# Kernel optimization log

Hardware: AMD Instinct MI355X
Metric: run time of the kernel (lower is better)

## Reference

```python
import jax, jax.numpy as jnp
import numpy as np

B, S, D, H = 2, 2048, 1024, 16
DK = D // H  # 64
THETA = 10000.0
SCALE = 1.0 / np.sqrt(DK)


def _rope(t, pos):
    """Apply rotary embedding. t: [b,h,s,dk], pos: [b,s] int."""
    inv_freq = THETA ** (-jnp.arange(0, DK, 2, dtype=jnp.float32) / DK)  # [dk/2]
    ang = pos[:, None, :, None].astype(jnp.float32) * inv_freq  # [b,1,s,dk/2]
    cos, sin = jnp.cos(ang), jnp.sin(ang)
    t1, t2 = t[..., 0::2], t[..., 1::2]  # interleaved pairs
    rot = jnp.stack([t1 * cos - t2 * sin, t1 * sin + t2 * cos], axis=-1)
    return rot.reshape(t.shape)


def setup_inputs() -> dict:
    key = jax.random.key(0)
    ks = jax.random.split(key, 9)
    sc = 0.02
    x = jax.random.normal(ks[0], (B, S, D), jnp.float32)
    token_position = jnp.tile(jnp.arange(S, dtype=jnp.int32)[None, :], (B, 1))
    Wq = jax.random.normal(ks[1], (D, D), jnp.float32) * sc
    Wk = jax.random.normal(ks[2], (D, D), jnp.float32) * sc
    Wv = jax.random.normal(ks[3], (D, D), jnp.float32) * sc
    Wo = jax.random.normal(ks[4], (D, D), jnp.float32) * sc
    bq = jnp.zeros((D,), jnp.float32)
    bk = jnp.zeros((D,), jnp.float32)
    bv = jnp.zeros((D,), jnp.float32)
    bo = jnp.zeros((D,), jnp.float32)
    return {"x": x, "token_position": token_position,
            "Wq": Wq, "bq": bq, "Wk": Wk, "bk": bk,
            "Wv": Wv, "bv": bv, "Wo": Wo, "bo": bo}


def reference(x, token_position, Wq, bq, Wk, bk, Wv, bv, Wo, bo):
    b, s, d = x.shape
    # projections, split heads: [b,s,d] -> [b,h,s,dk]
    def heads(t):
        return t.reshape(b, s, H, DK).transpose(0, 2, 1, 3)
    q = heads(x @ Wq + bq)
    k = heads(x @ Wk + bk)
    v = heads(x @ Wv + bv)
    q = _rope(q, token_position)
    k = _rope(k, token_position)
    scores = jnp.einsum('bhnk,bhmk->bhnm', q, k) * SCALE  # [b,h,s,s]
    causal = jnp.tril(jnp.ones((s, s), dtype=bool))
    scores = jnp.where(causal, scores, -jnp.inf)
    probs = jax.nn.softmax(scores, axis=-1)
    o = jnp.einsum('bhnm,bhmk->bhnk', probs, v)  # [b,h,s,dk]
    o = o.transpose(0, 2, 1, 3).reshape(b, s, d)
    return o @ Wo + bo
```

## Files before the change

kernel.cpp:

```cpp
#include <hip/hip_runtime.h>
#include <math.h>

#define BB  2
#define SS  2048
#define DD  1024
#define HH  16
#define DKK 64

constexpr float kScale = 0.125f;
constexpr float kC1 = 0.18033688011112042f;
constexpr float kC2 = 23.0831206542234144f;

typedef __bf16 bf16x8 __attribute__((ext_vector_type(8)));
typedef float f32x4 __attribute__((ext_vector_type(4)));

__device__ __forceinline__ void async_copy16(const void* g, void* l) {
  __builtin_amdgcn_global_load_lds(
      (const __attribute__((address_space(1))) void*)g,
      (__attribute__((address_space(3))) void*)l, 16, 0, 0);
}

__global__ __launch_bounds__(256) void prep_kernel(
    const float* __restrict__ x, const int* __restrict__ pos,
    const float* __restrict__ W0, const float* __restrict__ W1,
    const float* __restrict__ W2, const float* __restrict__ W3,
    __bf16* __restrict__ xb, float2* __restrict__ rtab,
    __bf16* __restrict__ T0, __bf16* __restrict__ T1,
    __bf16* __restrict__ T2, __bf16* __restrict__ T3) {
  __shared__ __bf16 tile[64][65];
  const int bid = blockIdx.x;
  const int t = threadIdx.x;
  if (bid < 2048) {
    const size_t i = ((size_t)bid * 256 + t) * 8;
    const float4 v0 = *(const float4*)(x + i);
    const float4 v1 = *(const float4*)(x + i + 4);
    bf16x8 o;
    o[0] = (__bf16)v0.x; o[1] = (__bf16)v0.y; o[2] = (__bf16)v0.z; o[3] = (__bf16)v0.w;
    o[4] = (__bf16)v1.x; o[5] = (__bf16)v1.y; o[6] = (__bf16)v1.z; o[7] = (__bf16)v1.w;
    *(bf16x8*)(xb + i) = o;
  } else if (bid < 2560) {
    const int idx = (bid - 2048) * 256 + t;
    const int m = idx >> 5, pi = idx & 31;
    const float inv = exp2f(-0.4152410118609203f * (float)pi);
    float sn, cs;
    __sincosf((float)pos[m] * inv, &sn, &cs);
    rtab[idx] = make_float2(cs, sn);
  } else {
    const int tid2 = bid - 2560;
    const int z = tid2 >> 8, rem = tid2 & 255;
    const float* W;
    __bf16* T;
    switch (z) {
      case 0: W = W0; T = T0; break;
      case 1: W = W1; T = T1; break;
      case 2: W = W2; T = T2; break;
      default: W = W3; T = T3; break;
    }
    const int k0 = (rem >> 4) * 64, n0 = (rem & 15) * 64;
    const int c = t & 63, rg = t >> 6;
#pragma unroll
    for (int i = 0; i < 16; i++) {
      const int r = rg + i * 4;
      tile[r][c] = (__bf16)W[(size_t)(k0 + r) * DD + n0 + c];
    }
    __syncthreads();
#pragma unroll
    for (int i = 0; i < 16; i++) {
      const int r = rg + i * 4;
      T[(size_t)(n0 + r) * DD + k0 + c] = tile[c][r];
    }
  }
}

__device__ __forceinline__ void gemm_core(
    const __bf16* __restrict__ A, const __bf16* __restrict__ Bt,
    int bm, int bn, f32x4 (&acc)[4][4], __bf16* As, __bf16* Bs) {
  const int t = threadIdx.x;
  const int lane = t & 63, wave = t >> 6;
  const int col = lane & 15, quad = lane >> 4;
  const int wm = (wave & 1) * 64, wn = (wave >> 1) * 64;
  const int r8 = lane >> 3;
  const int cg = (lane & 7) ^ r8;
  const __bf16* ag = A + (size_t)(bm + wave * 32 + r8) * DD + cg * 8;
  const __bf16* bg = Bt + (size_t)(bn + wave * 32 + r8) * DD + cg * 8;
  __bf16* asb = As + wave * 32 * 64;
  __bf16* bsb = Bs + wave * 32 * 64;

  for (int kt = 0; kt < DD; kt += 64) {
#pragma unroll
    for (int c = 0; c < 4; c++) {
      async_copy16(ag + (size_t)c * 8 * DD + kt, asb + c * 512);
      async_copy16(bg + (size_t)c * 8 * DD + kt, bsb + c * 512);
    }
    __syncthreads();
#pragma unroll
    for (int ks = 0; ks < 2; ks++) {
      bf16x8 af[4], bf[4];
#pragma unroll
      for (int i = 0; i < 4; i++)
        af[i] = *(const bf16x8*)(As + (wm + i * 16 + col) * 64 +
                                 (((ks * 4 + quad) ^ (col & 7)) * 8));
#pragma unroll
      for (int j = 0; j < 4; j++)
        bf[j] = *(const bf16x8*)(Bs + (wn + j * 16 + col) * 64 +
                                 (((ks * 4 + quad) ^ (col & 7)) * 8));
#pragma unroll
      for (int i = 0; i < 4; i++)
#pragma unroll
        for (int j = 0; j < 4; j++)
          acc[i][j] =
              __builtin_amdgcn_mfma_f32_16x16x32_bf16(af[i], bf[j], acc[i][j], 0, 0, 0);
    }
    __syncthreads();
  }
}

__global__ __launch_bounds__(256) void qkv_gemm_kernel(
    const __bf16* __restrict__ xb, const __bf16* __restrict__ WqT,
    const __bf16* __restrict__ WkT, const __bf16* __restrict__ WvT,
    const float* __restrict__ bq, const float* __restrict__ bk,
    const float* __restrict__ bv, const float2* __restrict__ ropetab,
    __bf16* __restrict__ qo, __bf16* __restrict__ ko, __bf16* __restrict__ vo) {
  __shared__ __bf16 As[128 * 64];
  __shared__ __bf16 Bs[128 * 64];
  const int mat = blockIdx.x >> 3;
  const int bn = (blockIdx.x & 7) * 128;
  const int bm = blockIdx.y * 128;

  f32x4 acc[4][4] = {};
  const int t = threadIdx.x, lane = t & 63, wave = t >> 6;
  const int col = lane & 15, quad = lane >> 4;
  const int wm = (wave & 1) * 64, wn = (wave >> 1) * 64;

  if (mat == 2) {
    gemm_core(WvT, xb, bn, bm, acc, As, Bs);
    const int b = bm >> 11;
#pragma unroll
    for (int i = 0; i < 4; i++) {
#pragma unroll
      for (int r = 0; r < 4; r++) {
        const int n = bn + wm + i * 16 + quad * 4 + r;
        const float bb = bv[n];
        const int h = n >> 6, dk = n & 63;
        __bf16* vrow = vo + ((size_t)(b * HH + h) * DKK + dk) * SS;
#pragma unroll
        for (int j = 0; j < 4; j++) {
          const int m = bm + wn + j * 16 + col;
          vrow[m & (SS - 1)] = (__bf16)(acc[i][j][r] + bb);
        }
      }
    }
    return;
  }

  const __bf16* Bt = mat == 0 ? WqT : WkT;
  const float* bias = mat == 0 ? bq : bk;
  __bf16* out = mat == 0 ? qo : ko;
  gemm_core(xb, Bt, bm, bn, acc, As, Bs);

#pragma unroll
  for (int i = 0; i < 4; i++) {
#pragma unroll
    for (int j = 0; j < 4; j++) {
      const int n = bn + wn + j * 16 + col;
      const float bb = bias[n];
      const int pi = (n & 63) >> 1;
#pragma unroll
      for (int r = 0; r < 4; r++) {
        const int m = bm + wm + i * 16 + quad * 4 + r;
        float v = acc[i][j][r] + bb;
        {
          const float other = __shfl_xor(v, 1, 64);
          const float2 cssn = ropetab[(size_t)m * 32 + pi];
          v = (n & 1) ? (other * cssn.y + v * cssn.x)
                      : (v * cssn.x - other * cssn.y);
        }
        const int h = n >> 6, dk = n & 63;
        const int b = m >> 11, s = m & (SS - 1);
        out[((size_t)(b * HH + h) * SS + s) * DKK + dk] = (__bf16)v;
      }
    }
  }
}

__global__ __launch_bounds__(256) void oproj_gemm_kernel(
    const __bf16* __restrict__ ob, const __bf16* __restrict__ WoT,
    const float* __restrict__ bo, float* __restrict__ out) {
  __shared__ __bf16 As[128 * 64];
  __shared__ __bf16 Bs[128 * 64];
  const int bn = blockIdx.x * 128;
  const int bm = blockIdx.y * 128;
  f32x4 acc[4][4] = {};
  gemm_core(ob, WoT, bm, bn, acc, As, Bs);

  const int t = threadIdx.x, lane = t & 63, wave = t >> 6;
  const int col = lane & 15, quad = lane >> 4;
  const int wm = (wave & 1) * 64, wn = (wave >> 1) * 64;
#pragma unroll
  for (int i = 0; i < 4; i++) {
#pragma unroll
    for (int j = 0; j < 4; j++) {
      const int n = bn + wn + j * 16 + col;
      const float bb = bo[n];
#pragma unroll
      for (int r = 0; r < 4; r++) {
        const int m = bm + wm + i * 16 + quad * 4 + r;
        out[(size_t)m * DD + n] = acc[i][j][r] + bb;
      }
    }
  }
}

__global__ __launch_bounds__(256) void flash_attn_mfma_kernel(
    const __bf16* __restrict__ q, const __bf16* __restrict__ k,
    const __bf16* __restrict__ vt, __bf16* __restrict__ o) {
  __shared__ __bf16 Ks[64 * 64];
  __shared__ __bf16 Vs[64 * 64];
  __shared__ __bf16 Ps[4][16 * 72];

  const int bh = blockIdx.x;
  const int pr = blockIdx.y;
  const int t = threadIdx.x, lane = t & 63, wave = t >> 6;
  const int col = lane & 15, quad = lane >> 4;
  const int r8 = lane >> 3;
  const int cg = (lane & 7) ^ r8;

  const __bf16* qb = q + (size_t)bh * SS * DKK;
  const __bf16* kb = k + (size_t)bh * SS * DKK;
  const __bf16* vtb = vt + (size_t)bh * DKK * SS;
  const int b = bh / HH, h = bh % HH;
  __bf16* pw = (__bf16*)Ps[wave];

#pragma unroll
  for (int phase = 0; phase < 2; phase++) {
    const int qt = phase == 0 ? pr : (31 - pr);
    const int rbase = qt * 64 + wave * 16;

    bf16x8 qf[2];
#pragma unroll
    for (int ks = 0; ks < 2; ks++)
      qf[ks] = *(const bf16x8*)(qb + (size_t)(rbase + col) * DKK + ks * 32 +
                                quad * 8);

    f32x4 oacc[4] = {};
    float l_lane[4] = {0.f, 0.f, 0.f, 0.f};

    for (int kt = 0; kt <= qt; kt++) {
#pragma unroll
      for (int i = 0; i < 2; i++) {
        const int slab = wave * 2 + i;
        async_copy16(kb + (size_t)(kt * 64 + slab * 8 + r8) * DKK + cg * 8,
                     Ks + slab * 512);
        async_copy16(vtb + (size_t)(slab * 8 + r8) * SS + kt * 64 + cg * 8,
                     Vs + slab * 512);
      }
      __syncthreads();

      f32x4 sc[4] = {};
#pragma unroll
      for (int ct = 0; ct < 4; ct++)
#pragma unroll
        for (int ks = 0; ks < 2; ks++) {
          const bf16x8 kf = *(const bf16x8*)(Ks + (ct * 16 + col) * 64 +
                                             (((ks * 4 + quad) ^ (col & 7)) * 8));
          sc[ct] = __builtin_amdgcn_mfma_f32_16x16x32_bf16(qf[ks], kf, sc[ct],
                                                           0, 0, 0);
        }

      const bool diag = (kt == qt);
#pragma unroll
      for (int ct = 0; ct < 4; ct++)
#pragma unroll
        for (int r = 0; r < 4; r++) {
          float p = exp2f(sc[ct][r] * kC1 - kC2);
          if (diag && (kt * 64 + ct * 16 + col) > (rbase + quad * 4 + r))
            p = 0.0f;
          l_lane[r] += p;
          pw[(quad * 4 + r) * 72 + ct * 16 + col] = (__bf16)p;
        }

      {
        bf16x8 pf[2];
#pragma unroll
        for (int ks = 0; ks < 2; ks++)
          pf[ks] = *(const bf16x8*)(pw + col * 72 + ks * 32 + quad * 8);
#pragma unroll
        for (int dt = 0; dt < 4; dt++)
#pragma unroll
          for (int ks = 0; ks < 2; ks++) {
            const bf16x8 vf = *(const bf16x8*)(Vs + (dt * 16 + col) * 64 +
                                               (((ks * 4 + quad) ^ (col & 7)) * 8));
            oacc[dt] = __builtin_amdgcn_mfma_f32_16x16x32_bf16(pf[ks], vf,
                                                               oacc[dt], 0, 0, 0);
          }
      }
      __syncthreads();
    }

#pragma unroll
    for (int r = 0; r < 4; r++) {
      float l = l_lane[r];
#pragma unroll
      for (int w = 1; w < 16; w <<= 1) l += __shfl_xor(l, w, 64);
      const float inv_l = 1.0f / l;
      const int s = rbase + quad * 4 + r;
#pragma unroll
      for (int dt = 0; dt < 4; dt++)
        o[((size_t)(b * SS + s) * HH + h) * DKK + dt * 16 + col] =
            (__bf16)(oacc[dt][r] * inv_l);
    }
  }
}

extern "C" void kernel_launch(void* const* d_in, const int* in_sizes, int n_in,
                              void* d_out, int out_size, void* d_ws,
                              size_t ws_size, hipStream_t stream) {
  const float* x  = (const float*)d_in[0];
  const int*  pos = (const int*)d_in[1];
  const float* Wq = (const float*)d_in[2];
  const float* bq = (const float*)d_in[3];
  const float* Wk = (const float*)d_in[4];
  const float* bk = (const float*)d_in[5];
  const float* Wv = (const float*)d_in[6];
  const float* bv = (const float*)d_in[7];
  const float* Wo = (const float*)d_in[8];
  const float* bo = (const float*)d_in[9];
  float* out = (float*)d_out;

  char* ws = (char*)d_ws;
  __bf16* xb  = (__bf16*)(ws);
  __bf16* WqT = (__bf16*)(ws + ((size_t)8  << 20));
  __bf16* WkT = (__bf16*)(ws + ((size_t)10 << 20));
  __bf16* WvT = (__bf16*)(ws + ((size_t)12 << 20));
  __bf16* WoT = (__bf16*)(ws + ((size_t)14 << 20));
  __bf16* qb  = (__bf16*)(ws + ((size_t)16 << 20));
  __bf16* kb  = (__bf16*)(ws + ((size_t)24 << 20));
  __bf16* vtb = (__bf16*)(ws + ((size_t)32 << 20));
  __bf16* ob  = (__bf16*)(ws + ((size_t)40 << 20));
  float2* rtab = (float2*)(ws + ((size_t)48 << 20));

  prep_kernel<<<3584, 256, 0, stream>>>(x, pos, Wq, Wk, Wv, Wo, xb, rtab, WqT,
                                        WkT, WvT, WoT);
  qkv_gemm_kernel<<<dim3(24, 32), 256, 0, stream>>>(xb, WqT, WkT, WvT, bq, bk,
                                                    bv, rtab, qb, kb, vtb);
  flash_attn_mfma_kernel<<<dim3(32, 16), 256, 0, stream>>>(qb, kb, vtb, ob);
  oproj_gemm_kernel<<<dim3(8, 32), 256, 0, stream>>>(ob, WoT, bo, out);
}
```

Before: 205.3 us.

## Double-buffer K/V tiles in flash attention and split paired query tiles into separate blocks

The attention kernel now prefetches the next K/V tile into a second LDS buffer while the current one is computed, which removes one barrier per iteration. The query-tile pairing loop is replaced by one block per query tile (grid 32x32), longest tiles first. The QK^T MFMA operands are swapped so each lane holds four consecutive key columns, which allows vectorized bf16x4 stores of P. Causal masking is limited to the diagonal sub-tile, and s_setprio is placed around MFMA sections. LDS use doubles, which may reduce occupancy, and the single-block grid gives up the built-in load balancing of the old pairing.

```diff
diff --git a/kernel.cpp b/kernel.cpp
--- a/kernel.cpp
+++ b/kernel.cpp
@@ -12,6 +12,7 @@
 constexpr float kC2 = 23.0831206542234144f;
 
 typedef __bf16 bf16x8 __attribute__((ext_vector_type(8)));
+typedef __bf16 bf16x4 __attribute__((ext_vector_type(4)));
 typedef float f32x4 __attribute__((ext_vector_type(4)));
 
 __device__ __forceinline__ void async_copy16(const void* g, void* l) {
@@ -214,12 +215,12 @@
 __global__ __launch_bounds__(256) void flash_attn_mfma_kernel(
     const __bf16* __restrict__ q, const __bf16* __restrict__ k,
     const __bf16* __restrict__ vt, __bf16* __restrict__ o) {
-  __shared__ __bf16 Ks[64 * 64];
-  __shared__ __bf16 Vs[64 * 64];
+  __shared__ __bf16 Ks[2][64 * 64];
+  __shared__ __bf16 Vs[2][64 * 64];
   __shared__ __bf16 Ps[4][16 * 72];
 
   const int bh = blockIdx.x;
-  const int pr = blockIdx.y;
+  const int qt = 31 - blockIdx.y;
   const int t = threadIdx.x, lane = t & 63, wave = t >> 6;
   const int col = lane & 15, quad = lane >> 4;
   const int r8 = lane >> 3;
@@ -231,84 +232,122 @@
   const int b = bh / HH, h = bh % HH;
   __bf16* pw = (__bf16*)Ps[wave];
 
-#pragma unroll
-  for (int phase = 0; phase < 2; phase++) {
-    const int qt = phase == 0 ? pr : (31 - pr);
-    const int rbase = qt * 64 + wave * 16;
-
-    bf16x8 qf[2];
-#pragma unroll
-    for (int ks = 0; ks < 2; ks++)
-      qf[ks] = *(const bf16x8*)(qb + (size_t)(rbase + col) * DKK + ks * 32 +
-                                quad * 8);
-
-    f32x4 oacc[4] = {};
-    float l_lane[4] = {0.f, 0.f, 0.f, 0.f};
-
-    for (int kt = 0; kt <= qt; kt++) {
-#pragma unroll
-      for (int i = 0; i < 2; i++) {
-        const int slab = wave * 2 + i;
-        async_copy16(kb + (size_t)(kt * 64 + slab * 8 + r8) * DKK + cg * 8,
-                     Ks + slab * 512);
-        async_copy16(vtb + (size_t)(slab * 8 + r8) * SS + kt * 64 + cg * 8,
-                     Vs + slab * 512);
-      }
-      __syncthreads();
-
-      f32x4 sc[4] = {};
-#pragma unroll
-      for (int ct = 0; ct < 4; ct++)
+  const int rbase = qt * 64 + wave * 16;
+
+  bf16x8 qf[2];
+#pragma unroll
+  for (int ks = 0; ks < 2; ks++)
+    qf[ks] = *(const bf16x8*)(qb + (size_t)(rbase + col) * DKK + ks * 32 +
+                              quad * 8);
+
+  f32x4 oacc[4] = {};
+  float l_lane = 0.f;
+
+  auto stage = [&](int kt, int buf) {
+#pragma unroll
+    for (int i = 0; i < 2; i++) {
+      const int slab = wave * 2 + i;
+      async_copy16(kb + (size_t)(kt * 64 + slab * 8 + r8) * DKK + cg * 8,
+                   &Ks[buf][slab * 512]);
+      async_copy16(vtb + (size_t)(slab * 8 + r8) * SS + kt * 64 + cg * 8,
+                   &Vs[buf][slab * 512]);
+    }
+  };
+
+  stage(0, 0);
+  __syncthreads();
+
+  int cur = 0;
+  for (int kt = 0; kt <= qt; kt++) {
+    if (kt < qt) stage(kt + 1, cur ^ 1);
+
+    f32x4 sc[4] = {};
+    __builtin_amdgcn_s_setprio(1);
+#pragma unroll
+    for (int ct = 0; ct < 4; ct++)
+#pragma unroll
+      for (int ks = 0; ks < 2; ks++) {
+        const bf16x8 kf = *(const bf16x8*)(&Ks[cur][(ct * 16 + col) * 64 +
+                                           (((ks * 4 + quad) ^ (col & 7)) * 8)]);
+        sc[ct] = __builtin_amdgcn_mfma_f32_16x16x32_bf16(kf, qf[ks], sc[ct],
+                                                         0, 0, 0);
+      }
+    __builtin_amdgcn_s_setprio(0);
+
+    if (kt < qt) {
+#pragma unroll
+      for (int ct = 0; ct < 4; ct++) {
+        float p0 = exp2f(sc[ct][0] * kC1 - kC2);
+        float p1 = exp2f(sc[ct][1] * kC1 - kC2);
+        float p2 = exp2f(sc[ct][2] * kC1 - kC2);
+        float p3 = exp2f(sc[ct][3] * kC1 - kC2);
+        l_lane += (p0 + p1) + (p2 + p3);
+        bf16x4 pv;
+        pv[0] = (__bf16)p0; pv[1] = (__bf16)p1;
+        pv[2] = (__bf16)p2; pv[3] = (__bf16)p3;
+        *(bf16x4*)(pw + col * 72 + ct * 16 + quad * 4) = pv;
+      }
+    } else {
+#pragma unroll
+      for (int ct = 0; ct < 4; ct++) {
+        bf16x4 pv;
+        if (ct > wave) {
+          pv[0] = pv[1] = pv[2] = pv[3] = (__bf16)0.0f;
+        } else if (ct < wave) {
+          float p0 = exp2f(sc[ct][0] * kC1 - kC2);
+          float p1 = exp2f(sc[ct][1] * kC1 - kC2);
+          float p2 = exp2f(sc[ct][2] * kC1 - kC2);
+          float p3 = exp2f(sc[ct][3] * kC1 - kC2);
+          l_lane += (p0 + p1) + (p2 + p3);
+          pv[0] = (__bf16)p0; pv[1] = (__bf16)p1;
+          pv[2] = (__bf16)p2; pv[3] = (__bf16)p3;
+        } else {
+#pragma unroll
+          for (int r = 0; r < 4; r++) {
+            float p = exp2f(sc[ct][r] * kC1 - kC2);
+            if (ct * 16 + quad * 4 + r > wave * 16 + col) p = 0.0f;
+            l_lane += p;
+            pv[r] = (__bf16)p;
+          }
+        }
+        *(bf16x4*)(pw + col * 72 + ct * 16 + quad * 4) = pv;
+      }
+    }
+
+    {
+      bf16x8 pf[2];
+#pragma unroll
+      for (int ks = 0; ks < 2; ks++)
+        pf[ks] = *(const bf16x8*)(pw + col * 72 + ks * 32 + quad * 8);
+      __builtin_amdgcn_s_setprio(1);
+#pragma unroll
+      for (int dt = 0; dt < 4; dt++)
 #pragma unroll
         for (int ks = 0; ks < 2; ks++) {
-          const bf16x8 kf = *(const bf16x8*)(Ks + (ct * 16 + col) * 64 +
-                                             (((ks * 4 + quad) ^ (col & 7)) * 8));
-          sc[ct] = __builtin_amdgcn_mfma_f32_16x16x32_bf16(qf[ks], kf, sc[ct],
-                                                           0, 0, 0);
+          const bf16x8 vf = *(const bf16x8*)(&Vs[cur][(dt * 16 + col) * 64 +
+                                             (((ks * 4 + quad) ^ (col & 7)) * 8)]);
+          oacc[dt] = __builtin_amdgcn_mfma_f32_16x16x32_bf16(pf[ks], vf,
+                                                             oacc[dt], 0, 0, 0);
         }
-
-      const bool diag = (kt == qt);
-#pragma unroll
-      for (int ct = 0; ct < 4; ct++)
-#pragma unroll
-        for (int r = 0; r < 4; r++) {
-          float p = exp2f(sc[ct][r] * kC1 - kC2);
-          if (diag && (kt * 64 + ct * 16 + col) > (rbase + quad * 4 + r))
-            p = 0.0f;
-          l_lane[r] += p;
-          pw[(quad * 4 + r) * 72 + ct * 16 + col] = (__bf16)p;
-        }
-
-      {
-        bf16x8 pf[2];
-#pragma unroll
-        for (int ks = 0; ks < 2; ks++)
-          pf[ks] = *(const bf16x8*)(pw + col * 72 + ks * 32 + quad * 8);
-#pragma unroll
-        for (int dt = 0; dt < 4; dt++)
-#pragma unroll
-          for (int ks = 0; ks < 2; ks++) {
-            const bf16x8 vf = *(const bf16x8*)(Vs + (dt * 16 + col) * 64 +
-                                               (((ks * 4 + quad) ^ (col & 7)) * 8));
-            oacc[dt] = __builtin_amdgcn_mfma_f32_16x16x32_bf16(pf[ks], vf,
-                                                               oacc[dt], 0, 0, 0);
-          }
-      }
-      __syncthreads();
-    }
-
-#pragma unroll
-    for (int r = 0; r < 4; r++) {
-      float l = l_lane[r];
-#pragma unroll
-      for (int w = 1; w < 16; w <<= 1) l += __shfl_xor(l, w, 64);
-      const float inv_l = 1.0f / l;
-      const int s = rbase + quad * 4 + r;
-#pragma unroll
-      for (int dt = 0; dt < 4; dt++)
-        o[((size_t)(b * SS + s) * HH + h) * DKK + dt * 16 + col] =
-            (__bf16)(oacc[dt][r] * inv_l);
-    }
+      __builtin_amdgcn_s_setprio(0);
+    }
+
+    __syncthreads();
+    cur ^= 1;
+  }
+
+  float l = l_lane;
+  l += __shfl_xor(l, 16, 64);
+  l += __shfl_xor(l, 32, 64);
+#pragma unroll
+  for (int r = 0; r < 4; r++) {
+    const float lr = __shfl(l, quad * 4 + r, 64);
+    const float inv_l = 1.0f / lr;
+    const int s = rbase + quad * 4 + r;
+#pragma unroll
+    for (int dt = 0; dt < 4; dt++)
+      o[((size_t)(b * SS + s) * HH + h) * DKK + dt * 16 + col] =
+          (__bf16)(oacc[dt][r] * inv_l);
   }
 }
 
@@ -343,6 +382,6 @@
                                         WkT, WvT, WoT);
   qkv_gemm_kernel<<<dim3(24, 32), 256, 0, stream>>>(xb, WqT, WkT, WvT, bq, bk,
                                                     bv, rtab, qb, kb, vtb);
-  flash_attn_mfma_kernel<<<dim3(32, 16), 256, 0, stream>>>(qb, kb, vtb, ob);
+  flash_attn_mfma_kernel<<<dim3(32, 32), 256, 0, stream>>>(qb, kb, vtb, ob);
   oproj_gemm_kernel<<<dim3(8, 32), 256, 0, stream>>>(ob, WoT, bo, out);
 }
```

Result: faster. 196.2 us (-4.4%).
